# Performance work log

Measured on AMD Instinct MI355X. Metric: run time of the kernel, lower is better.

## Reference

```python
import jax, jax.numpy as jnp
import numpy as np

B, T, V, H = 128, 1024, 256, 512  # batch, max seq len, vocab_count, latent_dim
PAD_VALUE = 0.0  # pad_index = 0 used as padding_value in pad_packed_sequence


def setup_inputs() -> dict:
    key = jax.random.key(0)
    k_x, k_len, k_wi, k_wh, k_bi, k_bh = jax.random.split(key, 6)
    x = jax.random.randint(k_x, (B, T), 0, V, dtype=jnp.int32)
    x_len = jax.random.randint(k_len, (B,), 1, T + 1, dtype=jnp.int32)
    x_len = x_len.at[0].set(T)  # ensure padded output length == T (static shape)
    s = 0.05
    W_ih = jax.random.normal(k_wi, (4 * H, V), dtype=jnp.float32) * s
    W_hh = jax.random.normal(k_wh, (4 * H, H), dtype=jnp.float32) * s
    b_ih = jax.random.normal(k_bi, (4 * H,), dtype=jnp.float32) * s
    b_hh = jax.random.normal(k_bh, (4 * H,), dtype=jnp.float32) * s
    return {"x": x, "x_len": x_len, "W_ih": W_ih, "W_hh": W_hh,
            "b_ih": b_ih, "b_hh": b_hh}


def _lstm_packed(x, x_len, W_ih, W_hh, b_ih, b_hh):
    # one-hot input projection (mathematically == embedding gather W_ih.T[x])
    oh = jax.nn.one_hot(x, W_ih.shape[1], dtype=W_ih.dtype)          # [B,T,V]
    proj = jnp.einsum('btv,gv->btg', oh, W_ih) + b_ih + b_hh         # [B,T,4H]
    proj_t = jnp.transpose(proj, (1, 0, 2))                          # [T,B,4H]
    # mask[t,b] = True while t < x_len[b] (packed-sequence semantics)
    mask_t = jnp.arange(proj.shape[1])[:, None] < x_len[None, :]     # [T,B]

    h0 = jnp.zeros((x.shape[0], W_hh.shape[1]), dtype=W_ih.dtype)
    c0 = jnp.zeros_like(h0)

    def step(carry, inp):
        h, c = carry
        p, m = inp                                                   # [B,4H],[B]
        gates = p + h @ W_hh.T
        i, f, g, o = jnp.split(gates, 4, axis=-1)                    # torch order i,f,g,o
        i = jax.nn.sigmoid(i)
        f = jax.nn.sigmoid(f)
        g = jnp.tanh(g)
        o = jax.nn.sigmoid(o)
        c_new = f * c + i * g
        h_new = o * jnp.tanh(c_new)
        m1 = m[:, None]
        h = jnp.where(m1, h_new, h)   # freeze state past each sequence's length
        c = jnp.where(m1, c_new, c)
        out = jnp.where(m1, h_new, PAD_VALUE)  # padding_value = pad_index
        return (h, c), out

    (h_T, c_T), ys = jax.lax.scan(step, (h0, c0), (proj_t, mask_t))
    output = jnp.transpose(ys, (1, 0, 2))                            # [B,T,H]
    return output, h_T, c_T


def reference(x, x_len, W_ih, W_hh, b_ih, b_hh):
    output, h_T, c_T = _lstm_packed(x, x_len, W_ih, W_hh, b_ih, b_hh)
    # hidden/cell shaped [num_layers*num_dirs=1, B, H] like torch LSTM
    return output, h_T[None], c_T[None]
```

## Files before the change

### kernel.cpp

```cpp
#include <hip/hip_runtime.h>
#include <hip/hip_bf16.h>


#define TT 1024
#define BB 128
#define HH 512
#define VV 256
#define NGP 8
#define GM 16
#define NWG 8
#define NE 64

typedef __attribute__((ext_vector_type(8))) short short8;
typedef __attribute__((ext_vector_type(4))) float f32x4;
typedef __attribute__((ext_vector_type(4))) unsigned u32x4;
typedef unsigned long long u64;
typedef unsigned short u16;
typedef unsigned char u8;
typedef unsigned u32;

__device__ __forceinline__ u16 f2bf(float f) {
  __hip_bfloat16 h = __float2bfloat16(f);
  return *reinterpret_cast<u16*>(&h);
}
__device__ __forceinline__ float sigm(float x) { return 1.0f / (1.0f + __expf(-x)); }
__device__ __forceinline__ float tanh_(float x) { return 1.0f - 2.0f / (1.0f + __expf(2.0f * x)); }

__global__ void lstm_init(const int* __restrict__ x, u8* __restrict__ x_t,
                          u32* __restrict__ hbuf) {
  int idx = blockIdx.x * 256 + threadIdx.x;
  int t = idx >> 7, b = idx & 127;
  x_t[idx] = (u8)x[b * TT + t];
  hbuf[idx] = 0u;
}

__launch_bounds__(256, 1)
__global__ void lstm_persist(const u8* __restrict__ x_t, const int* __restrict__ x_len,
                             const float* __restrict__ W_ih, const float* __restrict__ W_hh,
                             const float* __restrict__ b_ih, const float* __restrict__ b_hh,
                             float* __restrict__ out,
                             u32* __restrict__ hbuf) {
  const int tid = threadIdx.x;
  const int wave = tid >> 6, lane = tid & 63;
  const int nn = lane & 15, quad = lane >> 4;
  const int g = blockIdx.x >> 3, ig = blockIdx.x & 7;

  __shared__ u16 hA[GM * 520];
  __shared__ float gates_s[GM * 260];
  __shared__ int gmax_s;

  short8 bw[4][16];
#pragma unroll
  for (int s = 0; s < 4; s++) {
    const float* src = W_hh + (size_t)(wave * HH + ig * NE + s * 16 + nn) * HH + quad * 8;
#pragma unroll
    for (int kt = 0; kt < 16; kt++) {
      const float* p = src + kt * 32;
      short8 v;
#pragma unroll
      for (int j = 0; j < 8; j++) v[j] = (short)f2bf(p[j]);
      bw[s][kt] = v;
    }
  }

  const int bc = tid >> 4, e4 = (tid & 15) * 4;
  const int bglob = g * GM + bc;
  const int xl = x_len[bglob];
  float bias[4][4];
#pragma unroll
  for (int q = 0; q < 4; q++)
#pragma unroll
    for (int j = 0; j < 4; j++) {
      int grow = q * HH + ig * NE + e4 + j;
      bias[q][j] = b_ih[grow] + b_hh[grow];
    }
  float cst[4] = {0.f, 0.f, 0.f, 0.f}, hst[4] = {0.f, 0.f, 0.f, 0.f};

  if (tid == 0) gmax_s = 1;
  __syncthreads();
  if ((tid & 15) == 0) atomicMax(&gmax_s, xl);

  const int srow = tid >> 4, sc16 = tid & 15;
  const u64 hb = (u64)hbuf;
  const u64 crow_off = (u64)((size_t)(g * GM + srow) * 128 * 16);

  const u64 pub_off = (u64)(((size_t)bglob * 128 + ig * 16 + (tid & 15)) * 16);

  __syncthreads();
  const int gmax = gmax_s;

  for (int t = 0; t < gmax; ++t) {
    const int slot = t & 1;

    const int xv = (int)x_t[t * BB + bglob];
    float w[4][4];
#pragma unroll
    for (int q = 0; q < 4; q++)
#pragma unroll
      for (int j = 0; j < 4; j++)
        w[q][j] = W_ih[(size_t)(q * HH + ig * NE + e4 + j) * VV + xv] + bias[q][j];

    {
      const u64 rb = hb + (u64)((size_t)slot * BB * 128 * 16) + crow_off;
      u32x4 vv[8];
      unsigned need = 0xFFu;
      const unsigned tt = (unsigned)t;
      while (need) {
#pragma unroll
        for (int k = 0; k < 8; ++k)
          if (need & (1u << k)) {
            asm volatile("global_load_dwordx4 %0, %1, off sc1"
                         : "=v"(vv[k])
                         : "v"(rb + (u64)((k * 16 + sc16) * 16))
                         : "memory");
          }
        asm volatile("s_waitcnt vmcnt(0)" ::: "memory");
#pragma unroll
        for (int k = 0; k < 8; ++k)
          if (vv[k][1] >= tt && vv[k][3] >= tt) need &= ~(1u << k);
      }
#pragma unroll
      for (int k = 0; k < 8; ++k) {
        u64 hw = (u64)vv[k][0] | ((u64)vv[k][2] << 32);
        *reinterpret_cast<u64*>(&hA[srow * 520 + k * 64 + sc16 * 4]) = hw;
      }
    }
    __syncthreads();

    {
      f32x4 acc[4] = {{0,0,0,0},{0,0,0,0},{0,0,0,0},{0,0,0,0}};
      const u16* ap = hA + nn * 520 + quad * 8;
#pragma unroll
      for (int kt = 0; kt < 16; kt++) {
        short8 a = *(const short8*)(ap + kt * 32);
#pragma unroll
        for (int s = 0; s < 4; s++)
          acc[s] = __builtin_amdgcn_mfma_f32_16x16x32_bf16(a, bw[s][kt], acc[s], 0, 0, 0);
      }
#pragma unroll
      for (int s = 0; s < 4; s++)
#pragma unroll
        for (int r = 0; r < 4; r++)
          gates_s[(quad * 4 + r) * 260 + wave * NE + s * 16 + nn] = acc[s][r];
    }
    __syncthreads();

    {
      f32x4 G0 = *(const f32x4*)&gates_s[bc * 260 + 0 * NE + e4];
      f32x4 G1 = *(const f32x4*)&gates_s[bc * 260 + 1 * NE + e4];
      f32x4 G2 = *(const f32x4*)&gates_s[bc * 260 + 2 * NE + e4];
      f32x4 G3 = *(const f32x4*)&gates_s[bc * 260 + 3 * NE + e4];
      const bool act = (t < xl);
      f32x4 outv;
#pragma unroll
      for (int j = 0; j < 4; j++) {
        float gi = G0[j] + w[0][j];
        float gf = G1[j] + w[1][j];
        float gg = G2[j] + w[2][j];
        float go = G3[j] + w[3][j];
        float iv = sigm(gi), fv = sigm(gf), gv = tanh_(gg), ov = sigm(go);
        float cn = fv * cst[j] + iv * gv;
        float hn = ov * tanh_(cn);
        if (act) { cst[j] = cn; hst[j] = hn; }
        outv[j] = act ? hn : 0.0f;
      }
      __builtin_nontemporal_store(outv,
          (f32x4*)&out[((size_t)bglob * TT + t) * HH + ig * NE + e4]);
      u32x4 pub;
      pub[0] = (u32)f2bf(hst[0]) | ((u32)f2bf(hst[1]) << 16);
      pub[1] = (u32)(t + 1);
      pub[2] = (u32)f2bf(hst[2]) | ((u32)f2bf(hst[3]) << 16);
      pub[3] = (u32)(t + 1);
      u64 pa = hb + (u64)((size_t)(slot ^ 1) * BB * 128 * 16) + pub_off;
      asm volatile("global_store_dwordx4 %0, %1, off sc1"
                   :: "v"(pa), "v"(pub) : "memory");
    }
  }

  {
    f32x4 z = {0.f, 0.f, 0.f, 0.f};
    for (int t = gmax; t < TT; ++t)
      __builtin_nontemporal_store(z,
          (f32x4*)&out[((size_t)bglob * TT + t) * HH + ig * NE + e4]);
  }

  {
    f32x4 hv, cv;
#pragma unroll
    for (int j = 0; j < 4; j++) { hv[j] = hst[j]; cv[j] = cst[j]; }
    *(f32x4*)&out[(size_t)BB * TT * HH + (size_t)bglob * HH + ig * NE + e4] = hv;
    *(f32x4*)&out[(size_t)BB * TT * HH + (size_t)BB * HH + (size_t)bglob * HH + ig * NE + e4] = cv;
  }
}

extern "C" void kernel_launch(void* const* d_in, const int* in_sizes, int n_in,
                              void* d_out, int out_size, void* d_ws, size_t ws_size,
                              hipStream_t stream) {
  const int*   x     = (const int*)d_in[0];
  const int*   x_len = (const int*)d_in[1];
  const float* W_ih  = (const float*)d_in[2];
  const float* W_hh  = (const float*)d_in[3];
  const float* b_ih  = (const float*)d_in[4];
  const float* b_hh  = (const float*)d_in[5];
  float* out = (float*)d_out;

  char* ws = (char*)d_ws;
  u8*  x_t  = (u8*)ws;
  u32* hbuf = (u32*)(ws + 131072);

  lstm_init<<<512, 256, 0, stream>>>(x, x_t, hbuf);
  lstm_persist<<<64, 256, 0, stream>>>(x_t, x_len, W_ih, W_hh, b_ih, b_hh, out, hbuf);
}
```

Before: 5.462 ms.

## Prefetch next-step input projections and defer output stores off the critical path

The W_ih gather for step t+1 is now issued after the h-exchange barrier of step t, so its latency overlaps the MFMA work instead of preceding the spin-wait. The output store for step t is delayed and issued right after the next step's h loads, with the last one flushed after the loop. The spin loop now issues all loads before its first wait and only reissues the ones still pending. This is meant to shorten the serial per-step critical path between blocks, at the cost of extra registers and a reordered store sequence.

```diff
diff --git a/kernel.cpp b/kernel.cpp
--- a/kernel.cpp
+++ b/kernel.cpp
@@ -89,35 +89,50 @@
   __syncthreads();
   const int gmax = gmax_s;
 
+  float w[4][4];
+  {
+    const int xv = (int)x_t[0 * BB + bglob];
+#pragma unroll
+    for (int q = 0; q < 4; q++)
+#pragma unroll
+      for (int j = 0; j < 4; j++)
+        w[q][j] = W_ih[(size_t)(q * HH + ig * NE + e4 + j) * VV + xv] + bias[q][j];
+  }
+
+  f32x4 outc = {0.f, 0.f, 0.f, 0.f};
+  u64 outaddr = 0;
+
   for (int t = 0; t < gmax; ++t) {
     const int slot = t & 1;
-
-    const int xv = (int)x_t[t * BB + bglob];
-    float w[4][4];
-#pragma unroll
-    for (int q = 0; q < 4; q++)
-#pragma unroll
-      for (int j = 0; j < 4; j++)
-        w[q][j] = W_ih[(size_t)(q * HH + ig * NE + e4 + j) * VV + xv] + bias[q][j];
 
     {
       const u64 rb = hb + (u64)((size_t)slot * BB * 128 * 16) + crow_off;
       u32x4 vv[8];
+#pragma unroll
+      for (int k = 0; k < 8; ++k)
+        asm volatile("global_load_dwordx4 %0, %1, off sc1"
+                     : "=v"(vv[k])
+                     : "v"(rb + (u64)((k * 16 + sc16) * 16))
+                     : "memory");
+      if (t)
+        asm volatile("global_store_dwordx4 %0, %1, off nt"
+                     :: "v"(outaddr), "v"(outc) : "memory");
       unsigned need = 0xFFu;
       const unsigned tt = (unsigned)t;
-      while (need) {
+      while (true) {
+        asm volatile("s_waitcnt vmcnt(0)" ::: "memory");
 #pragma unroll
         for (int k = 0; k < 8; ++k)
-          if (need & (1u << k)) {
+          if ((need >> k) & 1)
+            if (vv[k][1] >= tt && vv[k][3] >= tt) need &= ~(1u << k);
+        if (!need) break;
+#pragma unroll
+        for (int k = 0; k < 8; ++k)
+          if ((need >> k) & 1)
             asm volatile("global_load_dwordx4 %0, %1, off sc1"
                          : "=v"(vv[k])
                          : "v"(rb + (u64)((k * 16 + sc16) * 16))
                          : "memory");
-          }
-        asm volatile("s_waitcnt vmcnt(0)" ::: "memory");
-#pragma unroll
-        for (int k = 0; k < 8; ++k)
-          if (vv[k][1] >= tt && vv[k][3] >= tt) need &= ~(1u << k);
       }
 #pragma unroll
       for (int k = 0; k < 8; ++k) {
@@ -127,6 +142,15 @@
     }
     __syncthreads();
 
+    float w2[4][4];
+    if (t + 1 < gmax) {
+      const int xv2 = (int)x_t[(t + 1) * BB + bglob];
+#pragma unroll
+      for (int q = 0; q < 4; q++)
+#pragma unroll
+        for (int j = 0; j < 4; j++)
+          w2[q][j] = W_ih[(size_t)(q * HH + ig * NE + e4 + j) * VV + xv2] + bias[q][j];
+    }
     {
       f32x4 acc[4] = {{0,0,0,0},{0,0,0,0},{0,0,0,0},{0,0,0,0}};
       const u16* ap = hA + nn * 520 + quad * 8;
@@ -164,8 +188,6 @@
         if (act) { cst[j] = cn; hst[j] = hn; }
         outv[j] = act ? hn : 0.0f;
       }
-      __builtin_nontemporal_store(outv,
-          (f32x4*)&out[((size_t)bglob * TT + t) * HH + ig * NE + e4]);
       u32x4 pub;
       pub[0] = (u32)f2bf(hst[0]) | ((u32)f2bf(hst[1]) << 16);
       pub[1] = (u32)(t + 1);
@@ -174,8 +196,18 @@
       u64 pa = hb + (u64)((size_t)(slot ^ 1) * BB * 128 * 16) + pub_off;
       asm volatile("global_store_dwordx4 %0, %1, off sc1"
                    :: "v"(pa), "v"(pub) : "memory");
-    }
-  }
+      outc = outv;
+      outaddr = (u64)&out[((size_t)bglob * TT + t) * HH + ig * NE + e4];
+    }
+    if (t + 1 < gmax) {
+#pragma unroll
+      for (int q = 0; q < 4; q++)
+#pragma unroll
+        for (int j = 0; j < 4; j++) w[q][j] = w2[q][j];
+    }
+  }
+
+  __builtin_nontemporal_store(outc, (f32x4*)outaddr);
 
   {
     f32x4 z = {0.f, 0.f, 0.f, 0.f};
```

Measured after the change: 6.030 ms. 1.1x slower.
